# Performance work log

Hardware: AMD Instinct MI355X
Metric: run time of the kernel (lower is better)

Reference implementation:

```python
import math
import jax, jax.numpy as jnp
import numpy as np

D_MODEL = 1024
N_HEADS = 16
D_K = D_MODEL // N_HEADS
THETA = 10000.0
B, S = 2, 2048


def setup_inputs() -> dict:
    key = jax.random.key(0)
    k1, k2, k3 = jax.random.split(key, 3)
    x = jax.random.normal(k1, (B, S, D_MODEL), dtype=jnp.float32)
    token_positions = jnp.arange(B * S, dtype=jnp.int32).reshape(B, S)
    std_qkv = math.sqrt(2.0 / (D_MODEL + 3 * D_MODEL))
    std_o = math.sqrt(2.0 / (D_MODEL + D_MODEL))
    W_qkv = jax.random.truncated_normal(k2, -3.0, 3.0, (3 * D_MODEL, D_MODEL), dtype=jnp.float32) * std_qkv
    W_o = jax.random.truncated_normal(k3, -3.0, 3.0, (D_MODEL, D_MODEL), dtype=jnp.float32) * std_o
    return {"x": x, "W_qkv": W_qkv, "W_o": W_o, "token_positions": token_positions}


def _rope(x, pos):
    # x: (B, H, S, D_K); pos: (B, S) int
    half = D_K // 2
    inv_freq = 1.0 / (THETA ** (jnp.arange(0, D_K, 2, dtype=jnp.float32) / D_K))  # (half,)
    # pos_extended = pos[:, None, :] -> freqs (B, 1, S, half)
    freqs = pos[:, None, :, None].astype(jnp.float32) * inv_freq
    cos, sin = jnp.cos(freqs), jnp.sin(freqs)
    xr = x.reshape(*x.shape[:-1], half, 2)
    x1, x2 = xr[..., 0], xr[..., 1]
    out = jnp.stack([x1 * cos - x2 * sin, x2 * cos + x1 * sin], axis=-1)
    return out.reshape(x.shape)


def reference(x, W_qkv, W_o, token_positions):
    seq_len = x.shape[-2]
    qkv = jnp.einsum('bsi,oi->bso', x, W_qkv)
    q, k, v = jnp.split(qkv, 3, axis=-1)
    # (B, S, H*D) -> (B, H, S, D)
    def to_heads(t):
        return t.reshape(t.shape[0], t.shape[1], N_HEADS, D_K).transpose(0, 2, 1, 3)
    q, k, v = to_heads(q), to_heads(k), to_heads(v)
    q = _rope(q, token_positions)
    k = _rope(k, token_positions)
    scores = jnp.einsum('bhnd,bhmd->bhnm', q, k) / math.sqrt(D_K)
    causal = jnp.tril(jnp.ones((seq_len, seq_len), dtype=bool))
    scores = jnp.where(causal, scores, -jnp.inf)
    attn = jax.nn.softmax(scores, axis=-1)
    out = jnp.einsum('bhnm,bhmd->bhnd', attn, v)
    out = out.transpose(0, 2, 1, 3).reshape(x.shape[0], seq_len, D_MODEL)
    return jnp.einsum('bsi,oi->bso', out, W_o)
```

## Files before the change

kernel.cpp:

```cpp
#include <hip/hip_runtime.h>
#include <cmath>

typedef __bf16 bf16;
typedef bf16 bf16x4 __attribute__((ext_vector_type(4)));
typedef bf16 bf16x8 __attribute__((ext_vector_type(8)));
typedef float f32x4 __attribute__((ext_vector_type(4)));

#define MFMA16(a, b, c) __builtin_amdgcn_mfma_f32_16x16x32_bf16(a, b, c, 0, 0, 0)

__global__ __launch_bounds__(256) void cvt_all(
    const float* __restrict__ x, const float* __restrict__ wqkv,
    const float* __restrict__ wo, bf16* __restrict__ xb,
    bf16* __restrict__ wqkvb, bf16* __restrict__ wob) {
  int i = (blockIdx.x * 256 + threadIdx.x) * 4;
  const float* src;
  bf16* dst;
  if (i < (4 << 20)) {
    src = x + i; dst = xb + i;
  } else if (i < (7 << 20)) {
    src = wqkv + (i - (4 << 20)); dst = wqkvb + (i - (4 << 20));
  } else {
    src = wo + (i - (7 << 20)); dst = wob + (i - (7 << 20));
  }
  const f32x4 v = *(const f32x4*)src;
  bf16x4 o = {(bf16)v[0], (bf16)v[1], (bf16)v[2], (bf16)v[3]};
  *(bf16x4*)dst = o;
}

template <int EPI>
__global__ __launch_bounds__(256) void gemm_nt(
    const bf16* __restrict__ A, const bf16* __restrict__ Bm,
    const int* __restrict__ tokpos,
    bf16* __restrict__ out0, bf16* __restrict__ out1, bf16* __restrict__ out2,
    float* __restrict__ outF, int N) {
  __shared__ __align__(16) bf16 As[2][128 * 32];
  __shared__ __align__(16) bf16 Bs[2][128 * 32];
  const int tid = threadIdx.x;
  const int w = tid >> 6, lane = tid & 63, quad = lane >> 4, m16 = lane & 15;
  const int m0 = blockIdx.y * 128, n0 = blockIdx.x * 128;
  const int wm = (w >> 1) * 64, wn = (w & 1) * 64;

  f32x4 acc[4][4] = {};

  const int row0 = tid >> 2, ch = tid & 3;
  const bf16* Ag0 = A + (size_t)(m0 + row0) * 1024 + ch * 8;
  const bf16* Ag1 = A + (size_t)(m0 + 64 + row0) * 1024 + ch * 8;
  const bf16* Bg0 = Bm + (size_t)(n0 + row0) * 1024 + ch * 8;
  const bf16* Bg1 = Bm + (size_t)(n0 + 64 + row0) * 1024 + ch * 8;

  bf16x8 ra0, ra1, rb0, rb1;
  auto LOAD = [&](int k0) {
    ra0 = *(const bf16x8*)(Ag0 + k0);
    ra1 = *(const bf16x8*)(Ag1 + k0);
    rb0 = *(const bf16x8*)(Bg0 + k0);
    rb1 = *(const bf16x8*)(Bg1 + k0);
  };
  auto WRITE = [&](int p) {
    *(bf16x8*)(As[p] + tid * 8) = ra0;
    *(bf16x8*)(As[p] + 2048 + tid * 8) = ra1;
    *(bf16x8*)(Bs[p] + tid * 8) = rb0;
    *(bf16x8*)(Bs[p] + 2048 + tid * 8) = rb1;
  };

  LOAD(0);
  WRITE(0);
  __syncthreads();

  int p = 0;
  for (int k0 = 0; k0 < 1024; k0 += 32) {
    const bool more = (k0 + 32) < 1024;
    if (more) LOAD(k0 + 32);
    bf16x8 af[4], bfr[4];
#pragma unroll
    for (int mi = 0; mi < 4; ++mi)
      af[mi] = *(const bf16x8*)(As[p] + (wm + mi * 16 + m16) * 32 + quad * 8);
#pragma unroll
    for (int ni = 0; ni < 4; ++ni)
      bfr[ni] = *(const bf16x8*)(Bs[p] + (wn + ni * 16 + m16) * 32 + quad * 8);
#pragma unroll
    for (int mi = 0; mi < 4; ++mi)
#pragma unroll
      for (int ni = 0; ni < 4; ++ni)
        acc[mi][ni] = MFMA16(af[mi], bfr[ni], acc[mi][ni]);
    if (more) {
      WRITE(1 - p);
      __syncthreads();
      p ^= 1;
    }
  }

  if constexpr (EPI == 0) {
#pragma unroll
    for (int mi = 0; mi < 4; ++mi) {
      int rowb = m0 + wm + mi * 16 + quad * 4;
#pragma unroll
      for (int r = 0; r < 4; ++r) {
        size_t off = (size_t)(rowb + r) * N + n0 + wn;
#pragma unroll
        for (int ni = 0; ni < 4; ++ni)
          outF[off + ni * 16 + m16] = acc[mi][ni][r];
      }
    }
  } else {
#pragma unroll
    for (int mi = 0; mi < 4; ++mi) {
      int rowb = m0 + wm + mi * 16 + quad * 4;
      int pos4[4];
#pragma unroll
      for (int r = 0; r < 4; ++r) pos4[r] = tokpos[rowb + r];
#pragma unroll
      for (int ni = 0; ni < 4; ++ni) {
        int col = n0 + wn + ni * 16 + m16;
        int sec = col >> 10, f = col & 1023, h = f >> 6, d = f & 63;
        if (sec == 2) {
#pragma unroll
          for (int r = 0; r < 4; ++r) {
            int row = rowb + r;
            int bb = row >> 11, s = row & 2047;
            out2[((size_t)(bb * 16 + h) * 64 + d) * 2048 + s] =
                (bf16)acc[mi][ni][r];
          }
        } else {
          float inv = __expf(-(float)(d & ~1) * (9.2103403719762f / 64.f));
          bf16* dst = sec ? out1 : out0;
          const float sc = sec ? 1.0f : 0.125f;
#pragma unroll
          for (int r = 0; r < 4; ++r) {
            float v = acc[mi][ni][r];
            float vp = __shfl_xor(v, 1);
            float ang = (float)pos4[r] * inv;
            float cs, sn;
            __sincosf(ang, &sn, &cs);
            float ov = (d & 1) ? (v * cs + vp * sn) : (v * cs - vp * sn);
            ov *= sc;
            int row = rowb + r;
            int bb = row >> 11, s = row & 2047;
            dst[((size_t)(bb * 16 + h) * 2048 + s) * 64 + d] = (bf16)ov;
          }
        }
      }
    }
  }
}

__global__ __launch_bounds__(256) void attn_kernel(
    const bf16* __restrict__ Q, const bf16* __restrict__ K,
    const bf16* __restrict__ Vt, bf16* __restrict__ O) {
  __shared__ __align__(16) bf16 KP[3][64 * 72];
  __shared__ __align__(16) bf16 VP[3][64 * 72];
  __shared__ __align__(16) bf16 PS[4][16 * 72];
  const int tid = threadIdx.x;
  const int w = tid >> 6, lane = tid & 63, quad = lane >> 4, m16 = lane & 15;
  const int bh = blockIdx.x;
  const int j = blockIdx.y;
  const int qtA = j, qtB = 31 - j;
  const int q0A = qtA * 64, q0B = qtB * 64;
  const bf16* Qb = Q + (size_t)bh * 2048 * 64;
  const bf16* Kb = K + (size_t)bh * 2048 * 64;
  const bf16* Vb = Vt + (size_t)bh * 64 * 2048;

  const int ch0 = w * 8, ch1 = (w + 4) * 8;
  const bf16* Kg = Kb + (size_t)lane * 64;
  const bf16* Vg = Vb + (size_t)lane * 2048;

  const bf16* qrowA = Qb + (size_t)(q0A + w * 16 + m16) * 64;
  const bf16* qrowB = Qb + (size_t)(q0B + w * 16 + m16) * 64;
  bf16x8 aqA[2], aqB[2];
  aqA[0] = *(const bf16x8*)(qrowA + quad * 8);
  aqA[1] = *(const bf16x8*)(qrowA + 32 + quad * 8);
  aqB[0] = *(const bf16x8*)(qrowB + quad * 8);
  aqB[1] = *(const bf16x8*)(qrowB + 32 + quad * 8);

  bf16x8 rk0, rk1, rv0, rv1;
  auto PREFETCH = [&](int kt) {
    rk0 = *(const bf16x8*)(Kg + (size_t)kt * 64 * 64 + ch0);
    rk1 = *(const bf16x8*)(Kg + (size_t)kt * 64 * 64 + ch1);
    rv0 = *(const bf16x8*)(Vg + kt * 64 + ch0);
    rv1 = *(const bf16x8*)(Vg + kt * 64 + ch1);
  };
  auto STAGE = [&](int p) {
    *(bf16x8*)(KP[p] + lane * 72 + ch0) = rk0;
    *(bf16x8*)(KP[p] + lane * 72 + ch1) = rk1;
    *(bf16x8*)(VP[p] + lane * 72 + ch0) = rv0;
    *(bf16x8*)(VP[p] + lane * 72 + ch1) = rv1;
  };

  PREFETCH(0);
  STAGE(0);
  PREFETCH(1);
  STAGE(1);
  __syncthreads();

  auto QK = [&](int p, const bf16x8* aq, f32x4* sa) {
#pragma unroll
    for (int kk = 0; kk < 2; ++kk)
#pragma unroll
      for (int ni = 0; ni < 4; ++ni) {
        bf16x8 bk = *(const bf16x8*)(KP[p] + (ni * 16 + m16) * 72 + kk * 32 +
                                     quad * 8);
        sa[ni] = MFMA16(aq[kk], bk, sa[ni]);
      }
  };

  f32x4 oA[4] = {}, oB[4] = {};
  float lA[4] = {0.f, 0.f, 0.f, 0.f}, lB[4] = {0.f, 0.f, 0.f, 0.f};
  const int qrel = w * 16 + quad * 4;

  auto SOFTPV = [&](int p, const f32x4* sa, f32x4* o, float* lp, bool diag) {
    bf16* ps = PS[w];
#pragma unroll
    for (int r = 0; r < 4; ++r) {
#pragma unroll
      for (int ni = 0; ni < 4; ++ni) {
        float pp = exp2f(fmaf(sa[ni][r], 1.44269504f, -11.5415603f));
        if (diag && (ni * 16 + m16) > qrel + r) pp = 0.f;
        lp[r] += pp;
        ps[(quad * 4 + r) * 72 + ni * 16 + m16] = (bf16)pp;
      }
    }
    bf16x8 ap[2];
    ap[0] = *(const bf16x8*)(ps + m16 * 72 + quad * 8);
    ap[1] = *(const bf16x8*)(ps + m16 * 72 + 32 + quad * 8);
#pragma unroll
    for (int kk = 0; kk < 2; ++kk)
#pragma unroll
      for (int ng = 0; ng < 4; ++ng) {
        bf16x8 bv = *(const bf16x8*)(VP[p] + (ng * 16 + m16) * 72 + kk * 32 +
                                     quad * 8);
        o[ng] = MFMA16(ap[kk], bv, o[ng]);
      }
  };

  f32x4 saA[4] = {}, saB[4] = {};
  QK(0, aqB, saB);
  QK(0, aqA, saA);

  int pc = 0, pn = 1, pst = 2;
  for (int kt = 0; kt <= qtB; ++kt) {
    const bool more = kt < qtB;
    const bool stage2 = (kt + 2) <= qtB;
    if (stage2) PREFETCH(kt + 2);

    f32x4 saBn[4] = {}, saAn[4] = {};
    if (more) QK(pn, aqB, saBn);
    if (kt + 1 <= qtA) QK(pn, aqA, saAn);

    SOFTPV(pc, saB, oB, lB, kt == qtB);
    if (kt <= qtA) SOFTPV(pc, saA, oA, lA, kt == qtA);

    if (stage2) STAGE(pst);
    if (more) __syncthreads();

#pragma unroll
    for (int i = 0; i < 4; ++i) { saB[i] = saBn[i]; saA[i] = saAn[i]; }
    int t = pc; pc = pn; pn = pst; pst = t;
  }

  const int b = bh >> 4, h = bh & 15;
  auto epilogue = [&](f32x4* o, float* lp, int q0) {
#pragma unroll
    for (int r = 0; r < 4; ++r) {
      float l = lp[r];
      l += __shfl_xor(l, 1);
      l += __shfl_xor(l, 2);
      l += __shfl_xor(l, 4);
      l += __shfl_xor(l, 8);
      float inv_l = 1.f / l;
      int s = q0 + w * 16 + quad * 4 + r;
      size_t rowoff = (size_t)(b * 2048 + s) * 1024 + h * 64;
#pragma unroll
      for (int ng = 0; ng < 4; ++ng)
        O[rowoff + ng * 16 + m16] = (bf16)(o[ng][r] * inv_l);
    }
  };
  epilogue(oA, lA, q0A);
  epilogue(oB, lB, q0B);
}

extern "C" void kernel_launch(void* const* d_in, const int* in_sizes, int n_in,
                              void* d_out, int out_size, void* d_ws, size_t ws_size,
                              hipStream_t stream) {
  (void)in_sizes; (void)n_in; (void)out_size; (void)ws_size;
  const float* x = (const float*)d_in[0];
  const float* Wqkv = (const float*)d_in[1];
  const float* Wo = (const float*)d_in[2];
  const int* tokpos = (const int*)d_in[3];
  float* out = (float*)d_out;

  const size_t NEL = (size_t)2 * 16 * 2048 * 64;
  bf16* Qws = (bf16*)d_ws;
  bf16* Kws = Qws + NEL;
  bf16* Vtw = Kws + NEL;
  bf16* Ows = Vtw + NEL;
  bf16* xb  = Ows + NEL;
  bf16* Wqkvb = xb + NEL;
  bf16* Wob = Wqkvb + (size_t)3072 * 1024;

  cvt_all<<<8192, 256, 0, stream>>>(x, Wqkv, Wo, xb, Wqkvb, Wob);

  gemm_nt<1><<<dim3(24, 32), 256, 0, stream>>>(xb, Wqkvb, tokpos, Qws, Kws,
                                               Vtw, nullptr, 3072);
  attn_kernel<<<dim3(32, 16), 256, 0, stream>>>(Qws, Kws, Vtw, Ows);
  gemm_nt<0><<<dim3(8, 32), 256, 0, stream>>>(Ows, Wob, nullptr, nullptr,
                                              nullptr, nullptr, out, 1024);
}
```

Measured before the change: 198.7 us.

## Stage GEMM tiles with direct global-to-LDS loads and narrow output-projection tiles

The GEMM kernel now fills shared memory with global_load_lds (16-byte direct-to-LDS loads) instead of loading into registers and then writing to LDS, which removes the register round trip and the separate LDS store step. The kernel is also templated on the N tile width, and the output projection uses a BN=64 tile. That doubles its grid to 512 blocks so more compute units are busy. Risks: the loads for the next stage are issued before the current compute, with only one barrier per iteration. Whether the async LDS writes to buffer p^1 are correctly ordered against readers of that buffer depends on barrier and vmcnt semantics.

```diff
diff --git a/kernel.cpp b/kernel.cpp
--- a/kernel.cpp
+++ b/kernel.cpp
@@ -7,6 +7,11 @@
 typedef float f32x4 __attribute__((ext_vector_type(4)));
 
 #define MFMA16(a, b, c) __builtin_amdgcn_mfma_f32_16x16x32_bf16(a, b, c, 0, 0, 0)
+
+#define GLOAD16(g, l)                                                   \
+  __builtin_amdgcn_global_load_lds(                                     \
+      (const __attribute__((address_space(1))) unsigned int*)(g),       \
+      (__attribute__((address_space(3))) unsigned int*)(l), 16, 0, 0)
 
 __global__ __launch_bounds__(256) void cvt_all(
     const float* __restrict__ x, const float* __restrict__ wqkv,
@@ -27,63 +32,55 @@
   *(bf16x4*)dst = o;
 }
 
-template <int EPI>
+template <int EPI, int BN>
 __global__ __launch_bounds__(256) void gemm_nt(
     const bf16* __restrict__ A, const bf16* __restrict__ Bm,
     const int* __restrict__ tokpos,
     bf16* __restrict__ out0, bf16* __restrict__ out1, bf16* __restrict__ out2,
     float* __restrict__ outF, int N) {
+  constexpr int NI = BN / 32;
   __shared__ __align__(16) bf16 As[2][128 * 32];
-  __shared__ __align__(16) bf16 Bs[2][128 * 32];
+  __shared__ __align__(16) bf16 Bs[2][BN * 32];
   const int tid = threadIdx.x;
   const int w = tid >> 6, lane = tid & 63, quad = lane >> 4, m16 = lane & 15;
-  const int m0 = blockIdx.y * 128, n0 = blockIdx.x * 128;
-  const int wm = (w >> 1) * 64, wn = (w & 1) * 64;
-
-  f32x4 acc[4][4] = {};
+  const int m0 = blockIdx.y * 128, n0 = blockIdx.x * BN;
+  const int wm = (w >> 1) * 64, wn = (w & 1) * (BN / 2);
+
+  f32x4 acc[4][NI] = {};
 
   const int row0 = tid >> 2, ch = tid & 3;
   const bf16* Ag0 = A + (size_t)(m0 + row0) * 1024 + ch * 8;
-  const bf16* Ag1 = A + (size_t)(m0 + 64 + row0) * 1024 + ch * 8;
+  const bf16* Ag1 = Ag0 + (size_t)64 * 1024;
   const bf16* Bg0 = Bm + (size_t)(n0 + row0) * 1024 + ch * 8;
-  const bf16* Bg1 = Bm + (size_t)(n0 + 64 + row0) * 1024 + ch * 8;
-
-  bf16x8 ra0, ra1, rb0, rb1;
-  auto LOAD = [&](int k0) {
-    ra0 = *(const bf16x8*)(Ag0 + k0);
-    ra1 = *(const bf16x8*)(Ag1 + k0);
-    rb0 = *(const bf16x8*)(Bg0 + k0);
-    rb1 = *(const bf16x8*)(Bg1 + k0);
-  };
-  auto WRITE = [&](int p) {
-    *(bf16x8*)(As[p] + tid * 8) = ra0;
-    *(bf16x8*)(As[p] + 2048 + tid * 8) = ra1;
-    *(bf16x8*)(Bs[p] + tid * 8) = rb0;
-    *(bf16x8*)(Bs[p] + 2048 + tid * 8) = rb1;
-  };
-
-  LOAD(0);
-  WRITE(0);
+  const bf16* Bg1 = Bg0 + (size_t)64 * 1024;
+
+  auto STAGE = [&](int p, int k0) {
+    GLOAD16(Ag0 + k0, &As[p][tid * 8]);
+    GLOAD16(Ag1 + k0, &As[p][2048 + tid * 8]);
+    GLOAD16(Bg0 + k0, &Bs[p][tid * 8]);
+    if constexpr (BN == 128) GLOAD16(Bg1 + k0, &Bs[p][2048 + tid * 8]);
+  };
+
+  STAGE(0, 0);
   __syncthreads();
 
   int p = 0;
   for (int k0 = 0; k0 < 1024; k0 += 32) {
     const bool more = (k0 + 32) < 1024;
-    if (more) LOAD(k0 + 32);
-    bf16x8 af[4], bfr[4];
+    if (more) STAGE(p ^ 1, k0 + 32);
+    bf16x8 af[4], bfr[NI];
 #pragma unroll
     for (int mi = 0; mi < 4; ++mi)
-      af[mi] = *(const bf16x8*)(As[p] + (wm + mi * 16 + m16) * 32 + quad * 8);
-#pragma unroll
-    for (int ni = 0; ni < 4; ++ni)
-      bfr[ni] = *(const bf16x8*)(Bs[p] + (wn + ni * 16 + m16) * 32 + quad * 8);
+      af[mi] = *(const bf16x8*)(&As[p][(wm + mi * 16 + m16) * 32 + quad * 8]);
+#pragma unroll
+    for (int ni = 0; ni < NI; ++ni)
+      bfr[ni] = *(const bf16x8*)(&Bs[p][(wn + ni * 16 + m16) * 32 + quad * 8]);
 #pragma unroll
     for (int mi = 0; mi < 4; ++mi)
 #pragma unroll
-      for (int ni = 0; ni < 4; ++ni)
+      for (int ni = 0; ni < NI; ++ni)
         acc[mi][ni] = MFMA16(af[mi], bfr[ni], acc[mi][ni]);
     if (more) {
-      WRITE(1 - p);
       __syncthreads();
       p ^= 1;
     }
@@ -97,7 +94,7 @@
       for (int r = 0; r < 4; ++r) {
         size_t off = (size_t)(rowb + r) * N + n0 + wn;
 #pragma unroll
-        for (int ni = 0; ni < 4; ++ni)
+        for (int ni = 0; ni < NI; ++ni)
           outF[off + ni * 16 + m16] = acc[mi][ni][r];
       }
     }
@@ -109,7 +106,7 @@
 #pragma unroll
       for (int r = 0; r < 4; ++r) pos4[r] = tokpos[rowb + r];
 #pragma unroll
-      for (int ni = 0; ni < 4; ++ni) {
+      for (int ni = 0; ni < NI; ++ni) {
         int col = n0 + wn + ni * 16 + m16;
         int sec = col >> 10, f = col & 1023, h = f >> 6, d = f & 63;
         if (sec == 2) {
@@ -298,9 +295,9 @@
 
   cvt_all<<<8192, 256, 0, stream>>>(x, Wqkv, Wo, xb, Wqkvb, Wob);
 
-  gemm_nt<1><<<dim3(24, 32), 256, 0, stream>>>(xb, Wqkvb, tokpos, Qws, Kws,
-                                               Vtw, nullptr, 3072);
+  gemm_nt<1, 128><<<dim3(24, 32), 256, 0, stream>>>(xb, Wqkvb, tokpos, Qws,
+                                                    Kws, Vtw, nullptr, 3072);
   attn_kernel<<<dim3(32, 16), 256, 0, stream>>>(Qws, Kws, Vtw, Ows);
-  gemm_nt<0><<<dim3(8, 32), 256, 0, stream>>>(Ows, Wob, nullptr, nullptr,
-                                              nullptr, nullptr, out, 1024);
+  gemm_nt<0, 64><<<dim3(16, 32), 256, 0, stream>>>(Ows, Wob, nullptr, nullptr,
+                                                   nullptr, nullptr, out, 1024);
 }
```

Measured after the change: 202.4 us. No clear change (+1.8%).
